# Performance work log

Hardware: AMD Instinct MI355X
Metric: run time of the kernel (lower is better)

The kernel has to match this reference:

```python
import jax, jax.numpy as jnp
import numpy as np
from jax import lax

DIM = 384
DIM_HEAD = 64
NUM_HEAD = DIM // DIM_HEAD
D_GROUPS = 3
NGD = DIM // D_GROUPS  # 128
KSIZE = 5
STRIDE = 2
PAD = KSIZE // 2
SCALE = DIM_HEAD ** -0.5
OFFSET_RANGE_FACTOR = 2.0
BN_EPS = 1e-6


def setup_inputs() -> dict:
    key = jax.random.key(0)
    ks = jax.random.split(key, 8)
    B, H, W = 8, 56, 56
    s = 0.02
    return {
        "x": jax.random.normal(ks[0], (B, DIM, H, W), jnp.float32),
        "q_w": jax.random.normal(ks[1], (DIM, DIM), jnp.float32) * s,
        "kv_w": jax.random.normal(ks[2], (2 * DIM, DIM), jnp.float32) * s,
        "proj_w": jax.random.normal(ks[3], (DIM, DIM), jnp.float32) * s,
        "proj_b": jnp.zeros((DIM,), jnp.float32),
        "dw_w": jax.random.normal(ks[4], (NGD, 1, KSIZE, KSIZE), jnp.float32) * s,
        "dw_b": jnp.zeros((NGD,), jnp.float32),
        "bn_w": jnp.ones((NGD,), jnp.float32),
        "bn_b": jnp.zeros((NGD,), jnp.float32),
        "bn_mean": jnp.zeros((NGD,), jnp.float32),
        "bn_var": jnp.ones((NGD,), jnp.float32),
        "pw_w": jax.random.normal(ks[5], (3, NGD), jnp.float32) * s,
    }


def grid_sample_bilinear(img, grid):
    # img: (N,C,H,W); grid: (N,Ho,Wo,2) with (x,y) in [-1,1]; align_corners=True, padding zeros
    N, C, H, W = img.shape
    gx = (grid[..., 0] + 1.0) * 0.5 * (W - 1)
    gy = (grid[..., 1] + 1.0) * 0.5 * (H - 1)
    x0 = jnp.floor(gx); y0 = jnp.floor(gy)
    x1 = x0 + 1.0; y1 = y0 + 1.0
    n_idx = jnp.arange(N)[:, None, None]

    def gather(yi, xi):
        valid = (yi >= 0) & (yi <= H - 1) & (xi >= 0) & (xi <= W - 1)
        yc = jnp.clip(yi, 0, H - 1).astype(jnp.int32)
        xc = jnp.clip(xi, 0, W - 1).astype(jnp.int32)
        v = img[n_idx, :, yc, xc]  # (N,Ho,Wo,C)
        return v * valid[..., None].astype(img.dtype)

    out = (gather(y0, x0) * ((x1 - gx) * (y1 - gy))[..., None]
           + gather(y1, x0) * ((x1 - gx) * (gy - y0))[..., None]
           + gather(y0, x1) * ((gx - x0) * (y1 - gy))[..., None]
           + gather(y1, x1) * ((gx - x0) * (gy - y0))[..., None])
    return out.transpose(0, 3, 1, 2)  # (N,C,Ho,Wo)


def _ref_points(H_off, W_off, n, dtype):
    ry = jnp.linspace(0.5, H_off - 0.5, H_off, dtype=dtype) / H_off * 2.0 - 1.0
    rx = jnp.linspace(0.5, W_off - 0.5, W_off, dtype=dtype) / W_off * 2.0 - 1.0
    ref = jnp.stack(jnp.meshgrid(ry, rx, indexing="ij"), -1)  # (Ho,Wo,2) as (y,x)
    return jnp.broadcast_to(ref[None], (n, H_off, W_off, 2))


def reference(x, q_w, kv_w, proj_w, proj_b, dw_w, dw_b, bn_w, bn_b, bn_mean, bn_var, pw_w):
    B, C, H, W = x.shape
    q = jnp.einsum("bchw,oc->bohw", x, q_w)  # 1x1 conv, no bias
    q_off = q.reshape(B * D_GROUPS, NGD, H, W)
    # depthwise conv (groups=NGD)
    off = lax.conv_general_dilated(q_off, dw_w, (STRIDE, STRIDE), [(PAD, PAD), (PAD, PAD)],
                                   feature_group_count=NGD,
                                   dimension_numbers=("NCHW", "OIHW", "NCHW"))
    off = off + dw_b[None, :, None, None]
    # BatchNorm2d (eval mode, running stats)
    off = (off - bn_mean[None, :, None, None]) * (bn_w / jnp.sqrt(bn_var + BN_EPS))[None, :, None, None] + bn_b[None, :, None, None]
    off = jax.nn.gelu(off, approximate=False)
    om = jnp.einsum("bchw,oc->bohw", off, pw_w)  # (Bg,3,Ho,Wo)
    offset, modulation = om[:, 0:2], jax.nn.sigmoid(om[:, 2:3])
    H_off, W_off = offset.shape[2], offset.shape[3]
    rng = jnp.array([1.0 / H_off, 1.0 / W_off], x.dtype).reshape(1, 2, 1, 1)
    offset = jnp.tanh(offset) * rng * OFFSET_RANGE_FACTOR
    offset = offset.transpose(0, 2, 3, 1)  # (Bg,Ho,Wo,2) as (y,x)
    pos = offset + _ref_points(H_off, W_off, B * D_GROUPS, x.dtype)
    grid = pos[..., ::-1]  # (x,y) for grid_sample
    x_s = grid_sample_bilinear(x.reshape(B * D_GROUPS, NGD, H, W), grid)
    x_s = x_s * jax.nn.sigmoid(modulation)  # note: double sigmoid as in source
    x_s = x_s.reshape(B, DIM, H_off, W_off)
    # attention
    qh = q.reshape(B, NUM_HEAD, DIM_HEAD, H * W).transpose(0, 1, 3, 2)  # (B,h,HW,d)
    kv = jnp.einsum("bchw,oc->bohw", x_s, kv_w)
    L = H_off * W_off
    kv = kv.reshape(B, 2, NUM_HEAD, DIM_HEAD, L).transpose(1, 0, 2, 4, 3)  # (2,B,h,L,d)
    k, v = kv[0], kv[1]
    attn = jax.nn.softmax(jnp.einsum("bhqd,bhkd->bhqk", qh, k) * SCALE, axis=-1)
    out = jnp.einsum("bhqk,bhkd->bhqd", attn, v)  # (B,h,HW,d)
    out = out.transpose(0, 1, 3, 2).reshape(B, DIM, H, W)
    out = jnp.einsum("bchw,oc->bohw", out, proj_w) + proj_b[None, :, None, None]
    return out
```

## Files before the change

### kernel.cpp

```cpp
#include <hip/hip_runtime.h>
#include <math.h>

#define DIMX 384
#define NHEAD 6
#define DHEAD 64
#define HW 3136
#define LKV 784
#define NGDX 128
#define NGRP 24

typedef __bf16 bf16_t;
typedef __bf16 bf16x4 __attribute__((ext_vector_type(4)));
typedef __bf16 bf16x8 __attribute__((ext_vector_type(8)));
typedef float  f32x4  __attribute__((ext_vector_type(4)));

typedef unsigned int u32_g __attribute__((address_space(1)));
typedef unsigned int u32_l __attribute__((address_space(3)));

static __device__ __forceinline__ f32x4 mfma16(bf16x8 a, bf16x8 b, f32x4 c) {
  return __builtin_amdgcn_mfma_f32_16x16x32_bf16(a, b, c, 0, 0, 0);
}
static __device__ __forceinline__ void gload16(const void* g, void* l) {
  __builtin_amdgcn_global_load_lds((const u32_g*)g, (u32_l*)l, 16, 0, 0);
}

__global__ __launch_bounds__(256) void xt_cvt(
    const float* __restrict__ x, bf16_t* __restrict__ xt)
{
  const int p0 = blockIdx.x * 64, c0 = blockIdx.y * 64, b = blockIdx.z;
  __shared__ float T[64][65];
  const int tid = threadIdx.x;
  {
    const int c = tid >> 2, pc = (tid & 3) * 16;
    const float* src = x + ((size_t)b * DIMX + c0 + c) * HW + p0 + pc;
#pragma unroll
    for (int j = 0; j < 4; ++j) {
      const float4 v = *(const float4*)(src + j * 4);
      T[c][pc + j * 4 + 0] = v.x; T[c][pc + j * 4 + 1] = v.y;
      T[c][pc + j * 4 + 2] = v.z; T[c][pc + j * 4 + 3] = v.w;
    }
  }
  __syncthreads();
  {
    const int p = tid >> 2, cc = (tid & 3) * 16;
    bf16_t* dst = xt + ((size_t)b * HW + p0 + p) * DIMX + c0 + cc;
#pragma unroll
    for (int jj = 0; jj < 2; ++jj) {
      bf16x8 o;
#pragma unroll
      for (int k = 0; k < 8; ++k) o[k] = (bf16_t)T[cc + jj * 8 + k][p];
      *(bf16x8*)(dst + jj * 8) = o;
    }
  }
}

__global__ __launch_bounds__(256) void cvt_w3(
    const float* __restrict__ qw, const float* __restrict__ kvw,
    const float* __restrict__ pw, bf16_t* __restrict__ dst)
{
  const int i = blockIdx.x * 256 + threadIdx.x;
  if (i >= 147456) return;
  const int e = i * 4;
  const float* src;
  int off;
  if (e < 147456)      { src = qw;  off = e; }
  else if (e < 442368) { src = kvw; off = e - 147456; }
  else                 { src = pw;  off = e - 442368; }
  const float4 v = *(const float4*)(src + off);
  bf16x4 o;
  o[0] = (bf16_t)v.x; o[1] = (bf16_t)v.y; o[2] = (bf16_t)v.z; o[3] = (bf16_t)v.w;
  *(bf16x4*)(dst + e) = o;
}

template<bool BIAS, bool OBF16>
__global__ __launch_bounds__(256) void gemm_qo(
    const bf16_t* __restrict__ W, const bf16_t* __restrict__ in,
    const float* __restrict__ bias, void* __restrict__ outv,
    int C, int P, int O)
{
  const int blk = blockIdx.x;
  const int y   = blk / 392;
  const int xb  = blk % 392;
  const int b   = xb / 49;
  const int o0  = y * 64;
  const int p0  = (xb % 49) * 64;
  __shared__ __align__(16) char smem[32768];
  const int tid = threadIdx.x;
  const int w = tid >> 6, lane = tid & 63, l15 = lane & 15, g = lane >> 4;
  const int lrow = lane >> 3;
  const int j    = lane & 7;

  const bf16_t* gA = W + (size_t)(o0 + w * 16 + lrow) * C + (j ^ lrow) * 8;
  const bf16_t* gB = in + ((size_t)b * P + p0 + w * 16 + lrow) * C + (j ^ lrow) * 8;

  f32x4 acc[4];
#pragma unroll
  for (int n = 0; n < 4; ++n) { acc[n][0]=0.f; acc[n][1]=0.f; acc[n][2]=0.f; acc[n][3]=0.f; }

  gload16(gA,         smem + w * 2048);
  gload16(gA + 8 * C, smem + w * 2048 + 1024);
  gload16(gB,         smem + 8192 + w * 2048);
  gload16(gB + 8 * C, smem + 8192 + w * 2048 + 1024);

  const int NK = C >> 6;
  for (int it = 0; it < NK; ++it) {
    const int buf = (it & 1) * 16384;
    __syncthreads();
    if (it + 1 < NK) {
      const int c1 = (it + 1) * 64;
      const int nb = ((it + 1) & 1) * 16384;
      gload16(gA + c1,         smem + nb + w * 2048);
      gload16(gA + c1 + 8 * C, smem + nb + w * 2048 + 1024);
      gload16(gB + c1,         smem + nb + 8192 + w * 2048);
      gload16(gB + c1 + 8 * C, smem + nb + 8192 + w * 2048 + 1024);
    }
#pragma unroll
    for (int ks = 0; ks < 2; ++ks) {
      const int cx = (ks * 64 + g * 16) ^ ((l15 & 7) << 4);
      const bf16x8 af = *(const bf16x8*)(smem + buf + (w * 16 + l15) * 128 + cx);
#pragma unroll
      for (int n = 0; n < 4; ++n) {
        const bf16x8 bfr = *(const bf16x8*)(smem + buf + 8192 + (n * 16 + l15) * 128 + cx);
        acc[n] = mfma16(af, bfr, acc[n]);
      }
    }
  }

  float badd[4];
#pragma unroll
  for (int r = 0; r < 4; ++r) badd[r] = BIAS ? bias[o0 + w * 16 + g * 4 + r] : 0.f;
#pragma unroll
  for (int n = 0; n < 4; ++n) {
    const int p = p0 + n * 16 + l15;
#pragma unroll
    for (int r = 0; r < 4; ++r) {
      const int o = o0 + w * 16 + g * 4 + r;
      const float v = acc[n][r] + badd[r];
      if (OBF16) ((bf16_t*)outv)[((size_t)b * O + o) * P + p] = (bf16_t)v;
      else       ((float*)outv)[((size_t)b * O + o) * P + p] = v;
    }
  }
}

__global__ __launch_bounds__(256) void gemm_kv(
    const bf16_t* __restrict__ W, const bf16_t* __restrict__ in,
    bf16_t* __restrict__ ktb, bf16_t* __restrict__ vtb, int C, int P, int O)
{
  const int b  = blockIdx.z;
  const int o0 = blockIdx.y * 64;
  const int p0 = blockIdx.x * 64;
  __shared__ __align__(16) bf16_t As[64][72];
  __shared__ __align__(16) bf16_t Bs[64][72];
  const int tid = threadIdx.x;
  const int w = tid >> 6, lane = tid & 63, l15 = lane & 15, g = lane >> 4;

  f32x4 acc[4];
#pragma unroll
  for (int n = 0; n < 4; ++n) { acc[n][0]=0.f; acc[n][1]=0.f; acc[n][2]=0.f; acc[n][3]=0.f; }

  for (int c0 = 0; c0 < C; c0 += 64) {
    {
      const int o = tid >> 2, cc = (tid & 3) * 16;
      const bf16_t* src = W + (size_t)(o0 + o) * C + c0 + cc;
      *(bf16x8*)&As[o][cc]     = *(const bf16x8*)src;
      *(bf16x8*)&As[o][cc + 8] = *(const bf16x8*)(src + 8);
    }
    {
      const int c = tid >> 2, pp = (tid & 3) * 16;
      const bf16_t* src = in + ((size_t)b * C + c0 + c) * P + p0 + pp;
#pragma unroll
      for (int jj = 0; jj < 2; ++jj) {
        bf16x8 v;
        if (p0 + pp + jj * 8 + 8 <= P) v = *(const bf16x8*)(src + jj * 8);
        else {
#pragma unroll
          for (int k = 0; k < 8; ++k) v[k] = (bf16_t)0.f;
        }
#pragma unroll
        for (int k = 0; k < 8; ++k) Bs[pp + jj * 8 + k][c] = v[k];
      }
    }
    __syncthreads();
#pragma unroll
    for (int ks = 0; ks < 2; ++ks) {
      const bf16x8 af = *(const bf16x8*)&As[w * 16 + l15][ks * 32 + g * 8];
#pragma unroll
      for (int n = 0; n < 4; ++n) {
        const bf16x8 bfr = *(const bf16x8*)&Bs[n * 16 + l15][ks * 32 + g * 8];
        acc[n] = mfma16(af, bfr, acc[n]);
      }
    }
    __syncthreads();
  }

  if (blockIdx.y < 6) {
    const int h = blockIdx.y;
#pragma unroll
    for (int n = 0; n < 4; ++n) {
      const int l = p0 + n * 16 + l15;
      if (l < P) {
        bf16x4 kq;
#pragma unroll
        for (int r = 0; r < 4; ++r) kq[r] = (bf16_t)acc[n][r];
        *(bf16x4*)&ktb[(((size_t)b * NHEAD + h) * LKV + l) * DHEAD + w * 16 + g * 4] = kq;
      }
    }
  } else {
#pragma unroll
    for (int n = 0; n < 4; ++n) {
      const int p = p0 + n * 16 + l15;
      if (p < P) {
#pragma unroll
        for (int r = 0; r < 4; ++r) {
          const int c = o0 - DIMX + w * 16 + g * 4 + r;
          vtb[((size_t)b * DIMX + c) * LKV + p] = (bf16_t)acc[n][r];
        }
      }
    }
  }
}

__global__ __launch_bounds__(256) void dw_bn_gelu(
    const bf16_t* __restrict__ q, const float* __restrict__ dw_w,
    const float* __restrict__ dw_b, const float* __restrict__ bn_w,
    const float* __restrict__ bn_b, const float* __restrict__ bn_mean,
    const float* __restrict__ bn_var, float* __restrict__ off)
{
  __shared__ float pl[3136];
  const int nc = blockIdx.x;
  const int c  = nc & 127;
  const bf16_t* plane = q + (size_t)nc * HW;
  const int tid = threadIdx.x;

  for (int i = tid; i < 392; i += 256) {
    const bf16x8 v = *(const bf16x8*)(plane + i * 8);
    f32x4 a, bq;
#pragma unroll
    for (int k = 0; k < 4; ++k) { a[k] = (float)v[k]; bq[k] = (float)v[4 + k]; }
    *(f32x4*)&pl[i * 8]     = a;
    *(f32x4*)&pl[i * 8 + 4] = bq;
  }
  float w[25];
#pragma unroll
  for (int k = 0; k < 25; ++k) w[k] = dw_w[c * 25 + k];
  const float beta  = dw_b[c];
  const float scale = bn_w[c] * rsqrtf(bn_var[c] + 1e-6f);
  const float shift = bn_b[c] - bn_mean[c] * scale;
  __syncthreads();

  for (int p = tid; p < LKV; p += 256) {
    const int oy = p / 28, ox = p % 28;
    const int iy0 = oy * 2 - 2, ix0 = ox * 2 - 2;
    float s = 0.f;
#pragma unroll
    for (int ky = 0; ky < 5; ++ky) {
      const int y = iy0 + ky;
      if ((unsigned)y >= 56u) continue;
#pragma unroll
      for (int kx = 0; kx < 5; ++kx) {
        const int x = ix0 + kx;
        if ((unsigned)x >= 56u) continue;
        s += pl[y * 56 + x] * w[ky * 5 + kx];
      }
    }
    s = (s + beta) * scale + shift;
    const float g = 0.5f * s * (1.f + erff(s * 0.70710678118654752f));
    off[(size_t)nc * LKV + p] = g;
  }
}

__global__ __launch_bounds__(64) void om_grid(
    const float* __restrict__ off, const float* __restrict__ pw_w,
    float* __restrict__ gxy, float* __restrict__ modb)
{
  const int n  = blockIdx.y;
  const int lane = threadIdx.x;
  const int p  = blockIdx.x * 16 + (lane & 15);
  const int cs = lane >> 4;
  const float* base = off + (size_t)n * NGDX * LKV + p;
  float s0 = 0.f, s1 = 0.f, s2 = 0.f;
#pragma unroll 8
  for (int cc = 0; cc < 32; ++cc) {
    const int c = cs * 32 + cc;
    const float v = base[(size_t)c * LKV];
    s0 += v * pw_w[c];
    s1 += v * pw_w[128 + c];
    s2 += v * pw_w[256 + c];
  }
  s0 += __shfl_xor(s0, 16); s0 += __shfl_xor(s0, 32);
  s1 += __shfl_xor(s1, 16); s1 += __shfl_xor(s1, 32);
  s2 += __shfl_xor(s2, 16); s2 += __shfl_xor(s2, 32);
  if (cs == 0) {
    const float sig1 = 1.f / (1.f + expf(-s2));
    const float mod  = 1.f / (1.f + expf(-sig1));
    const float offy = tanhf(s0) * (2.f / 28.f);
    const float offx = tanhf(s1) * (2.f / 28.f);
    const int i = p / 28, j = p % 28;
    const float refy = ((i + 0.5f) / 28.f) * 2.f - 1.f;
    const float refx = ((j + 0.5f) / 28.f) * 2.f - 1.f;
    const float gy = (offy + refy + 1.f) * 0.5f * 55.f;
    const float gx = (offx + refx + 1.f) * 0.5f * 55.f;
    gxy[((size_t)n * LKV + p) * 2 + 0] = gx;
    gxy[((size_t)n * LKV + p) * 2 + 1] = gy;
    modb[(size_t)n * LKV + p] = mod;
  }
}

__global__ __launch_bounds__(256) void sample_mod(
    const float* __restrict__ x, const float* __restrict__ gxy,
    const float* __restrict__ modb, bf16_t* __restrict__ xs)
{
  const int nc = blockIdx.x;
  const int n  = nc >> 7;
  const float* img = x + (size_t)nc * HW;
  for (int p = threadIdx.x; p < LKV; p += 256) {
    const float gx = gxy[((size_t)n * LKV + p) * 2 + 0];
    const float gy = gxy[((size_t)n * LKV + p) * 2 + 1];
    const float x0f = floorf(gx), y0f = floorf(gy);
    const float wx1 = gx - x0f, wy1 = gy - y0f;
    const float wx0 = (x0f + 1.f) - gx, wy0 = (y0f + 1.f) - gy;
    const int ix0 = (int)x0f, iy0 = (int)y0f;
    const int ix1 = ix0 + 1,  iy1 = iy0 + 1;
    const bool vx0 = (ix0 >= 0) && (ix0 < 56), vx1 = (ix1 >= 0) && (ix1 < 56);
    const bool vy0 = (iy0 >= 0) && (iy0 < 56), vy1 = (iy1 >= 0) && (iy1 < 56);
    const int cx0 = min(max(ix0, 0), 55), cx1 = min(max(ix1, 0), 55);
    const int cy0 = min(max(iy0, 0), 55), cy1 = min(max(iy1, 0), 55);
    const float f00 = (vy0 && vx0) ? img[cy0 * 56 + cx0] : 0.f;
    const float f10 = (vy1 && vx0) ? img[cy1 * 56 + cx0] : 0.f;
    const float f01 = (vy0 && vx1) ? img[cy0 * 56 + cx1] : 0.f;
    const float f11 = (vy1 && vx1) ? img[cy1 * 56 + cx1] : 0.f;
    const float v = f00 * (wx0 * wy0) + f10 * (wx0 * wy1)
                  + f01 * (wx1 * wy0) + f11 * (wx1 * wy1);
    xs[(size_t)nc * LKV + p] = (bf16_t)(v * modb[(size_t)n * LKV + p]);
  }
}

__global__ __launch_bounds__(256, 3) void attn_mfma(
    const bf16_t* __restrict__ q, const bf16_t* __restrict__ kt,
    const bf16_t* __restrict__ vt, bf16_t* __restrict__ aot)
{
  const int blk = blockIdx.x;
  const int bh  = blk % 48;
  const int t25 = blk / 48;
  const int h   = bh % NHEAD;
  const int b   = bh / NHEAD;
  const int p0  = t25 * 128;

  __shared__ __align__(16) char smem[40960];
  float (*Os)[68] = (float (*)[68])(smem);

  const int tid  = threadIdx.x;
  const int w    = tid >> 6;
  const int lane = tid & 63;
  const int l15  = lane & 15;
  const int g    = lane >> 4;
  const int lrow = lane >> 3;
  const int j    = lane & 7;

  const bf16_t* qb = q  + (size_t)(b * DIMX + h * DHEAD) * HW;
  const bf16_t* kb = kt + ((size_t)(b * NHEAD + h) * LKV) * DHEAD;
  const bf16_t* vb = vt + (size_t)(b * DIMX + h * DHEAD) * LKV;

  const bf16_t* gK = kb + (size_t)(w * 16 + lrow) * DHEAD + (j ^ lrow) * 8;
  const bf16_t* gV = vb + (size_t)(w * 16 + lrow) * LKV + (j ^ lrow) * 8;

  const float QSCL = 0.18033688011112042f;
  bf16x8 qf[2][2];
#pragma unroll
  for (int rs = 0; rs < 2; ++rs) {
    const int p = p0 + w * 32 + rs * 16 + l15;
    const bool valid = p < HW;
#pragma unroll
    for (int c2 = 0; c2 < 2; ++c2)
#pragma unroll
      for (int i = 0; i < 8; ++i) {
        const int d = c2 * 32 + g * 8 + i;
        qf[rs][c2][i] = valid ? (bf16_t)((float)qb[(size_t)d * HW + p] * QSCL) : (bf16_t)0.f;
      }
  }
  bf16x8 ones;
#pragma unroll
  for (int i = 0; i < 8; ++i) ones[i] = (bf16_t)1.0f;

  f32x4 acc[2][4];
  f32x4 lacc[2];
#pragma unroll
  for (int rs = 0; rs < 2; ++rs) {
    lacc[rs][0]=0.f; lacc[rs][1]=0.f; lacc[rs][2]=0.f; lacc[rs][3]=0.f;
#pragma unroll
    for (int n = 0; n < 4; ++n) { acc[rs][n][0]=0.f; acc[rs][n][1]=0.f; acc[rs][n][2]=0.f; acc[rs][n][3]=0.f; }
  }

  gload16(gK,                    smem + w * 2048);
  gload16(gK + (size_t)8*DHEAD,  smem + w * 2048 + 1024);
  gload16(gV,                    smem + 8192 + w * 2048);
  gload16(gV + (size_t)8*LKV,    smem + 8192 + w * 2048 + 1024);

  for (int t = 0; t < 13; ++t) {
    const int l0  = t * 64;
    const int buf = (t & 1) * 16384;
    __syncthreads();
    if (t < 12) {
      const int l1 = t * 64 + 64;
      const int nb = ((t + 1) & 1) * 16384;
      gload16(gK + (size_t)l1 * DHEAD,       smem + nb + w * 2048);
      gload16(gK + (size_t)(l1 + 8) * DHEAD, smem + nb + w * 2048 + 1024);
      gload16(gV + l1,                       smem + nb + 8192 + w * 2048);
      gload16(gV + (size_t)8 * LKV + l1,     smem + nb + 8192 + w * 2048 + 1024);
    }

    f32x4 s[2][4];
    __builtin_amdgcn_s_setprio(1);
#pragma unroll
    for (int n = 0; n < 4; ++n) {
      const int row = n * 16 + l15;
      const int cx0 = (g * 16) ^ ((l15 & 7) << 4);
      const int cx1 = (64 + g * 16) ^ ((l15 & 7) << 4);
      const bf16x8 k0 = *(const bf16x8*)(smem + buf + row * 128 + cx0);
      const bf16x8 k1 = *(const bf16x8*)(smem + buf + row * 128 + cx1);
#pragma unroll
      for (int rs = 0; rs < 2; ++rs) {
        f32x4 z; z[0]=0.f; z[1]=0.f; z[2]=0.f; z[3]=0.f;
        z = mfma16(k0, qf[rs][0], z);
        z = mfma16(k1, qf[rs][1], z);
        s[rs][n] = z;
      }
    }
    __builtin_amdgcn_s_setprio(0);
    if (l0 + 64 > LKV) {
#pragma unroll
      for (int n = 0; n < 4; ++n)
#pragma unroll
        for (int r = 0; r < 4; ++r)
          if (l0 + n * 16 + g * 4 + r >= LKV) {
#pragma unroll
            for (int rs = 0; rs < 2; ++rs) s[rs][n][r] = -1e30f;
          }
    }

    const int prow  = w * 16 + l15;
    char* pbase = smem + 32768 + prow * 128;
#pragma unroll
    for (int rs = 0; rs < 2; ++rs) {
#pragma unroll
      for (int n = 0; n < 4; ++n) {
        bf16x4 pk;
#pragma unroll
        for (int r = 0; r < 4; ++r) pk[r] = (bf16_t)exp2f(s[rs][n][r]);
        *(bf16x4*)(pbase + ((n * 32 + g * 8) ^ ((l15 & 7) << 4))) = pk;
      }
      __builtin_amdgcn_s_setprio(1);
#pragma unroll
      for (int c2 = 0; c2 < 2; ++c2) {
        bf16x8 vf[4];
#pragma unroll
        for (int n = 0; n < 4; ++n) {
          const int row = n * 16 + l15;
          const int cx = (c2 * 64 + g * 16) ^ ((l15 & 7) << 4);
          vf[n] = *(const bf16x8*)(smem + 8192 + buf + row * 128 + cx);
        }
        const bf16x8 pf = *(const bf16x8*)(pbase + ((c2 * 64 + g * 16) ^ ((l15 & 7) << 4)));
        lacc[rs] = mfma16(ones, pf, lacc[rs]);
#pragma unroll
        for (int n = 0; n < 4; ++n)
          acc[rs][n] = mfma16(vf[n], pf, acc[rs][n]);
      }
      __builtin_amdgcn_s_setprio(0);
    }
  }
  __syncthreads();

#pragma unroll
  for (int rs = 0; rs < 2; ++rs) {
    const float inv = 1.f / lacc[rs][0];
#pragma unroll
    for (int n = 0; n < 4; ++n) {
      f32x4 o4;
#pragma unroll
      for (int r = 0; r < 4; ++r) o4[r] = acc[rs][n][r] * inv;
      *(f32x4*)&Os[w * 32 + rs * 16 + l15][n * 16 + g * 4] = o4;
    }
  }
  __syncthreads();
  {
    const int pr = tid >> 1, c0 = (tid & 1) * 32;
    const int p = p0 + pr;
    if (p < HW) {
      bf16_t* dst = aot + ((size_t)b * HW + p) * DIMX + h * DHEAD + c0;
#pragma unroll
      for (int jj = 0; jj < 4; ++jj) {
        const f32x4 a = *(const f32x4*)&Os[pr][c0 + jj * 8];
        const f32x4 bq = *(const f32x4*)&Os[pr][c0 + jj * 8 + 4];
        bf16x8 o8;
        o8[0]=(bf16_t)a[0]; o8[1]=(bf16_t)a[1]; o8[2]=(bf16_t)a[2]; o8[3]=(bf16_t)a[3];
        o8[4]=(bf16_t)bq[0]; o8[5]=(bf16_t)bq[1]; o8[6]=(bf16_t)bq[2]; o8[7]=(bf16_t)bq[3];
        *(bf16x8*)(dst + jj * 8) = o8;
      }
    }
  }
}

extern "C" void kernel_launch(void* const* d_in, const int* in_sizes, int n_in,
                              void* d_out, int out_size, void* d_ws, size_t ws_size,
                              hipStream_t stream) {
  const float* x       = (const float*)d_in[0];
  const float* q_w     = (const float*)d_in[1];
  const float* kv_w    = (const float*)d_in[2];
  const float* proj_w  = (const float*)d_in[3];
  const float* proj_b  = (const float*)d_in[4];
  const float* dw_w    = (const float*)d_in[5];
  const float* dw_b    = (const float*)d_in[6];
  const float* bn_w    = (const float*)d_in[7];
  const float* bn_b    = (const float*)d_in[8];
  const float* bn_mean = (const float*)d_in[9];
  const float* bn_var  = (const float*)d_in[10];
  const float* pw_w    = (const float*)d_in[11];
  float* out = (float*)d_out;

  char* ws = (char*)d_ws;
  bf16_t* qbufb = (bf16_t*)(ws);
  float*  offb  = (float*)(ws + 19267584);
  float*  gxy   = (float*)(ws + 28901376);
  float*  modb  = (float*)(ws + 29051904);
  bf16_t* ktb   = (bf16_t*)(ws + 29127168);
  bf16_t* vtb   = (bf16_t*)(ws + 33944064);
  bf16_t* xsb   = (bf16_t*)(ws + 38760960);
  bf16_t* xt    = (bf16_t*)(ws + 43577856);
  bf16_t* aot   = xt;
  bf16_t* wbf   = (bf16_t*)(ws + 62845440);
  bf16_t* q_wb  = wbf;
  bf16_t* kv_wb = wbf + 147456;
  bf16_t* pj_wb = wbf + 442368;

  const dim3 blk(256);
  xt_cvt<<<dim3(49, 6, 8), blk, 0, stream>>>(x, xt);
  cvt_w3<<<dim3(576), blk, 0, stream>>>(q_w, kv_w, proj_w, wbf);
  gemm_qo<false, true><<<dim3(2352), blk, 0, stream>>>(q_wb, xt, nullptr, qbufb, 384, 3136, 384);
  dw_bn_gelu<<<dim3(3072), blk, 0, stream>>>(qbufb, dw_w, dw_b, bn_w, bn_b, bn_mean, bn_var, offb);
  om_grid<<<dim3(49, 24), dim3(64), 0, stream>>>(offb, pw_w, gxy, modb);
  sample_mod<<<dim3(3072), blk, 0, stream>>>(x, gxy, modb, xsb);
  gemm_kv<<<dim3(13, 12, 8), blk, 0, stream>>>(kv_wb, xsb, ktb, vtb, 384, 784, 768);
  attn_mfma<<<dim3(1200), blk, 0, stream>>>(qbufb, ktb, vtb, aot);
  gemm_qo<true, false><<<dim3(2352), blk, 0, stream>>>(pj_wb, aot, proj_b, out, 384, 3136, 384);
}
```

Baseline: 160.4 us.

## Double attention block to 512 threads sharing K/V tiles; pad depthwise conv plane

The attention kernel now runs 512-thread blocks that each cover 256 query positions, so every K/V tile loaded into shared memory serves twice as many queries. This halves global K/V traffic per query and halves the grid size. The output staging now takes two passes through the Os buffer, and shared memory grows to 48KB. Separately, the depthwise conv stages a zero-padded 60x60 plane in shared memory, which removes the per-tap bounds checks at the cost of an extra zeroing pass and a second barrier.

```diff
diff --git a/kernel.cpp b/kernel.cpp
--- a/kernel.cpp
+++ b/kernel.cpp
@@ -226,20 +226,13 @@
     const float* __restrict__ bn_b, const float* __restrict__ bn_mean,
     const float* __restrict__ bn_var, float* __restrict__ off)
 {
-  __shared__ float pl[3136];
+  __shared__ float pl[3600];
   const int nc = blockIdx.x;
   const int c  = nc & 127;
   const bf16_t* plane = q + (size_t)nc * HW;
   const int tid = threadIdx.x;
 
-  for (int i = tid; i < 392; i += 256) {
-    const bf16x8 v = *(const bf16x8*)(plane + i * 8);
-    f32x4 a, bq;
-#pragma unroll
-    for (int k = 0; k < 4; ++k) { a[k] = (float)v[k]; bq[k] = (float)v[4 + k]; }
-    *(f32x4*)&pl[i * 8]     = a;
-    *(f32x4*)&pl[i * 8 + 4] = bq;
-  }
+  for (int i = tid; i < 3600; i += 256) pl[i] = 0.f;
   float w[25];
 #pragma unroll
   for (int k = 0; k < 25; ++k) w[k] = dw_w[c * 25 + k];
@@ -248,21 +241,23 @@
   const float shift = bn_b[c] - bn_mean[c] * scale;
   __syncthreads();
 
+  for (int i = tid; i < 392; i += 256) {
+    const bf16x8 v = *(const bf16x8*)(plane + i * 8);
+    const int y = i / 7, x0 = (i % 7) * 8;
+    float* dst = &pl[(y + 2) * 60 + 2 + x0];
+#pragma unroll
+    for (int k = 0; k < 8; ++k) dst[k] = (float)v[k];
+  }
+  __syncthreads();
+
   for (int p = tid; p < LKV; p += 256) {
     const int oy = p / 28, ox = p % 28;
-    const int iy0 = oy * 2 - 2, ix0 = ox * 2 - 2;
     float s = 0.f;
 #pragma unroll
-    for (int ky = 0; ky < 5; ++ky) {
-      const int y = iy0 + ky;
-      if ((unsigned)y >= 56u) continue;
-#pragma unroll
-      for (int kx = 0; kx < 5; ++kx) {
-        const int x = ix0 + kx;
-        if ((unsigned)x >= 56u) continue;
-        s += pl[y * 56 + x] * w[ky * 5 + kx];
-      }
-    }
+    for (int ky = 0; ky < 5; ++ky)
+#pragma unroll
+      for (int kx = 0; kx < 5; ++kx)
+        s += pl[(oy * 2 + ky) * 60 + ox * 2 + kx] * w[ky * 5 + kx];
     s = (s + beta) * scale + shift;
     const float g = 0.5f * s * (1.f + erff(s * 0.70710678118654752f));
     off[(size_t)nc * LKV + p] = g;
@@ -335,7 +330,7 @@
   }
 }
 
-__global__ __launch_bounds__(256, 3) void attn_mfma(
+__global__ __launch_bounds__(512, 4) void attn_mfma(
     const bf16_t* __restrict__ q, const bf16_t* __restrict__ kt,
     const bf16_t* __restrict__ vt, bf16_t* __restrict__ aot)
 {
@@ -344,9 +339,9 @@
   const int t25 = blk / 48;
   const int h   = bh % NHEAD;
   const int b   = bh / NHEAD;
-  const int p0  = t25 * 128;
-
-  __shared__ __align__(16) char smem[40960];
+  const int p0  = t25 * 256;
+
+  __shared__ __align__(16) char smem[49152];
   float (*Os)[68] = (float (*)[68])(smem);
 
   const int tid  = threadIdx.x;
@@ -361,8 +356,8 @@
   const bf16_t* kb = kt + ((size_t)(b * NHEAD + h) * LKV) * DHEAD;
   const bf16_t* vb = vt + (size_t)(b * DIMX + h * DHEAD) * LKV;
 
-  const bf16_t* gK = kb + (size_t)(w * 16 + lrow) * DHEAD + (j ^ lrow) * 8;
-  const bf16_t* gV = vb + (size_t)(w * 16 + lrow) * LKV + (j ^ lrow) * 8;
+  const bf16_t* gK = kb + (size_t)(w * 8 + lrow) * DHEAD + (j ^ lrow) * 8;
+  const bf16_t* gV = vb + (size_t)(w * 8 + lrow) * LKV + (j ^ lrow) * 8;
 
   const float QSCL = 0.18033688011112042f;
   bf16x8 qf[2][2];
@@ -391,22 +386,18 @@
     for (int n = 0; n < 4; ++n) { acc[rs][n][0]=0.f; acc[rs][n][1]=0.f; acc[rs][n][2]=0.f; acc[rs][n][3]=0.f; }
   }
 
-  gload16(gK,                    smem + w * 2048);
-  gload16(gK + (size_t)8*DHEAD,  smem + w * 2048 + 1024);
-  gload16(gV,                    smem + 8192 + w * 2048);
-  gload16(gV + (size_t)8*LKV,    smem + 8192 + w * 2048 + 1024);
+  gload16(gK, smem + w * 1024);
+  gload16(gV, smem + 8192 + w * 1024);
 
   for (int t = 0; t < 13; ++t) {
     const int l0  = t * 64;
     const int buf = (t & 1) * 16384;
     __syncthreads();
     if (t < 12) {
-      const int l1 = t * 64 + 64;
+      const int l1 = l0 + 64;
       const int nb = ((t + 1) & 1) * 16384;
-      gload16(gK + (size_t)l1 * DHEAD,       smem + nb + w * 2048);
-      gload16(gK + (size_t)(l1 + 8) * DHEAD, smem + nb + w * 2048 + 1024);
-      gload16(gV + l1,                       smem + nb + 8192 + w * 2048);
-      gload16(gV + (size_t)8 * LKV + l1,     smem + nb + 8192 + w * 2048 + 1024);
+      gload16(gK + (size_t)l1 * DHEAD, smem + nb + w * 1024);
+      gload16(gV + l1,                 smem + nb + 8192 + w * 1024);
     }
 
     f32x4 s[2][4];
@@ -438,8 +429,7 @@
           }
     }
 
-    const int prow  = w * 16 + l15;
-    char* pbase = smem + 32768 + prow * 128;
+    char* pbase = smem + 32768 + (w * 16 + l15) * 128;
 #pragma unroll
     for (int rs = 0; rs < 2; ++rs) {
 #pragma unroll
@@ -470,33 +460,41 @@
   }
   __syncthreads();
 
-#pragma unroll
-  for (int rs = 0; rs < 2; ++rs) {
-    const float inv = 1.f / lacc[rs][0];
-#pragma unroll
-    for (int n = 0; n < 4; ++n) {
-      f32x4 o4;
-#pragma unroll
-      for (int r = 0; r < 4; ++r) o4[r] = acc[rs][n][r] * inv;
-      *(f32x4*)&Os[w * 32 + rs * 16 + l15][n * 16 + g * 4] = o4;
-    }
-  }
-  __syncthreads();
-  {
-    const int pr = tid >> 1, c0 = (tid & 1) * 32;
-    const int p = p0 + pr;
-    if (p < HW) {
-      bf16_t* dst = aot + ((size_t)b * HW + p) * DIMX + h * DHEAD + c0;
-#pragma unroll
-      for (int jj = 0; jj < 4; ++jj) {
-        const f32x4 a = *(const f32x4*)&Os[pr][c0 + jj * 8];
-        const f32x4 bq = *(const f32x4*)&Os[pr][c0 + jj * 8 + 4];
-        bf16x8 o8;
-        o8[0]=(bf16_t)a[0]; o8[1]=(bf16_t)a[1]; o8[2]=(bf16_t)a[2]; o8[3]=(bf16_t)a[3];
-        o8[4]=(bf16_t)bq[0]; o8[5]=(bf16_t)bq[1]; o8[6]=(bf16_t)bq[2]; o8[7]=(bf16_t)bq[3];
-        *(bf16x8*)(dst + jj * 8) = o8;
-      }
-    }
+  const int wl    = w & 3;
+  const int whalf = w >> 2;
+#pragma unroll
+  for (int pass = 0; pass < 2; ++pass) {
+    if (whalf == pass) {
+#pragma unroll
+      for (int rs = 0; rs < 2; ++rs) {
+        const float inv = 1.f / lacc[rs][0];
+#pragma unroll
+        for (int n = 0; n < 4; ++n) {
+          f32x4 o4;
+#pragma unroll
+          for (int r = 0; r < 4; ++r) o4[r] = acc[rs][n][r] * inv;
+          *(f32x4*)&Os[wl * 32 + rs * 16 + l15][n * 16 + g * 4] = o4;
+        }
+      }
+    }
+    __syncthreads();
+    {
+      const int pr = tid >> 2, c0 = (tid & 3) * 16;
+      const int p = p0 + pass * 128 + pr;
+      if (p < HW) {
+        bf16_t* dst = aot + ((size_t)b * HW + p) * DIMX + h * DHEAD + c0;
+#pragma unroll
+        for (int jj = 0; jj < 2; ++jj) {
+          const f32x4 a = *(const f32x4*)&Os[pr][c0 + jj * 8];
+          const f32x4 bq = *(const f32x4*)&Os[pr][c0 + jj * 8 + 4];
+          bf16x8 o8;
+          o8[0]=(bf16_t)a[0]; o8[1]=(bf16_t)a[1]; o8[2]=(bf16_t)a[2]; o8[3]=(bf16_t)a[3];
+          o8[4]=(bf16_t)bq[0]; o8[5]=(bf16_t)bq[1]; o8[6]=(bf16_t)bq[2]; o8[7]=(bf16_t)bq[3];
+          *(bf16x8*)(dst + jj * 8) = o8;
+        }
+      }
+    }
+    __syncthreads();
   }
 }
 
@@ -540,6 +538,6 @@
   om_grid<<<dim3(49, 24), dim3(64), 0, stream>>>(offb, pw_w, gxy, modb);
   sample_mod<<<dim3(3072), blk, 0, stream>>>(x, gxy, modb, xsb);
   gemm_kv<<<dim3(13, 12, 8), blk, 0, stream>>>(kv_wb, xsb, ktb, vtb, 384, 784, 768);
-  attn_mfma<<<dim3(1200), blk, 0, stream>>>(qbufb, ktb, vtb, aot);
+  attn_mfma<<<dim3(624), dim3(512), 0, stream>>>(qbufb, ktb, vtb, aot);
   gemm_qo<true, false><<<dim3(2352), blk, 0, stream>>>(pj_wb, aot, proj_b, out, 384, 3136, 384);
 }
```

Result: no change. 161.6 us (+0.8%).

## Fuse fp32-to-bf16 transpose of x into Q GEMM and pad depthwise conv plane

Applied to the files above, without the earlier changes.

Removes the separate xt_cvt kernel: the Q projection GEMM now reads fp32 x directly, converts it to bf16 and transposes it into shared memory per tile. This drops one kernel launch and a full write and read of the transposed bf16 copy of x. The new GEMM is not double-buffered and does scattered 2-byte LDS stores, so its inner loop may be slower, and each weight-row block re-reads and re-converts the fp32 x tile. Separately, the depthwise conv stages a zero-padded 60-wide plane so the 5x5 stencil loop needs no bounds checks.

```diff
diff --git a/kernel.cpp b/kernel.cpp
--- a/kernel.cpp
+++ b/kernel.cpp
@@ -22,36 +22,6 @@
 }
 static __device__ __forceinline__ void gload16(const void* g, void* l) {
   __builtin_amdgcn_global_load_lds((const u32_g*)g, (u32_l*)l, 16, 0, 0);
-}
-
-__global__ __launch_bounds__(256) void xt_cvt(
-    const float* __restrict__ x, bf16_t* __restrict__ xt)
-{
-  const int p0 = blockIdx.x * 64, c0 = blockIdx.y * 64, b = blockIdx.z;
-  __shared__ float T[64][65];
-  const int tid = threadIdx.x;
-  {
-    const int c = tid >> 2, pc = (tid & 3) * 16;
-    const float* src = x + ((size_t)b * DIMX + c0 + c) * HW + p0 + pc;
-#pragma unroll
-    for (int j = 0; j < 4; ++j) {
-      const float4 v = *(const float4*)(src + j * 4);
-      T[c][pc + j * 4 + 0] = v.x; T[c][pc + j * 4 + 1] = v.y;
-      T[c][pc + j * 4 + 2] = v.z; T[c][pc + j * 4 + 3] = v.w;
-    }
-  }
-  __syncthreads();
-  {
-    const int p = tid >> 2, cc = (tid & 3) * 16;
-    bf16_t* dst = xt + ((size_t)b * HW + p0 + p) * DIMX + c0 + cc;
-#pragma unroll
-    for (int jj = 0; jj < 2; ++jj) {
-      bf16x8 o;
-#pragma unroll
-      for (int k = 0; k < 8; ++k) o[k] = (bf16_t)T[cc + jj * 8 + k][p];
-      *(bf16x8*)(dst + jj * 8) = o;
-    }
-  }
 }
 
 __global__ __launch_bounds__(256) void cvt_w3(
@@ -72,10 +42,73 @@
   *(bf16x4*)(dst + e) = o;
 }
 
-template<bool BIAS, bool OBF16>
+__global__ __launch_bounds__(256) void gemm_q(
+    const bf16_t* __restrict__ W, const float* __restrict__ x,
+    bf16_t* __restrict__ outq)
+{
+  const int C = DIMX, P = HW, O = DIMX;
+  const int blk = blockIdx.x;
+  const int y   = blk / 392;
+  const int xb  = blk % 392;
+  const int b   = xb / 49;
+  const int o0  = y * 64;
+  const int p0  = (xb % 49) * 64;
+  __shared__ __align__(16) char smemA[8192];
+  __shared__ __align__(16) bf16_t Bs[64][72];
+  const int tid = threadIdx.x;
+  const int w = tid >> 6, lane = tid & 63, l15 = lane & 15, g = lane >> 4;
+  const int lrow = lane >> 3;
+  const int j    = lane & 7;
+
+  const bf16_t* gA = W + (size_t)(o0 + w * 16 + lrow) * C + (j ^ lrow) * 8;
+
+  f32x4 acc[4];
+#pragma unroll
+  for (int n = 0; n < 4; ++n) { acc[n][0]=0.f; acc[n][1]=0.f; acc[n][2]=0.f; acc[n][3]=0.f; }
+
+  for (int c0 = 0; c0 < C; c0 += 64) {
+    gload16(gA + c0,         smemA + w * 2048);
+    gload16(gA + c0 + 8 * C, smemA + w * 2048 + 1024);
+    {
+      const int c = tid >> 2, pp = (tid & 3) * 16;
+      const float* src = x + ((size_t)b * C + c0 + c) * HW + p0 + pp;
+#pragma unroll
+      for (int q4 = 0; q4 < 4; ++q4) {
+        const float4 v = *(const float4*)(src + q4 * 4);
+        Bs[pp + q4 * 4 + 0][c] = (bf16_t)v.x;
+        Bs[pp + q4 * 4 + 1][c] = (bf16_t)v.y;
+        Bs[pp + q4 * 4 + 2][c] = (bf16_t)v.z;
+        Bs[pp + q4 * 4 + 3][c] = (bf16_t)v.w;
+      }
+    }
+    __syncthreads();
+#pragma unroll
+    for (int ks = 0; ks < 2; ++ks) {
+      const int cx = (ks * 64 + g * 16) ^ ((l15 & 7) << 4);
+      const bf16x8 af = *(const bf16x8*)(smemA + (w * 16 + l15) * 128 + cx);
+#pragma unroll
+      for (int n = 0; n < 4; ++n) {
+        const bf16x8 bfr = *(const bf16x8*)&Bs[n * 16 + l15][ks * 32 + g * 8];
+        acc[n] = mfma16(af, bfr, acc[n]);
+      }
+    }
+    __syncthreads();
+  }
+
+#pragma unroll
+  for (int n = 0; n < 4; ++n) {
+    const int p = p0 + n * 16 + l15;
+#pragma unroll
+    for (int r = 0; r < 4; ++r) {
+      const int o = o0 + w * 16 + g * 4 + r;
+      outq[((size_t)b * O + o) * P + p] = (bf16_t)acc[n][r];
+    }
+  }
+}
+
 __global__ __launch_bounds__(256) void gemm_qo(
     const bf16_t* __restrict__ W, const bf16_t* __restrict__ in,
-    const float* __restrict__ bias, void* __restrict__ outv,
+    const float* __restrict__ bias, float* __restrict__ out,
     int C, int P, int O)
 {
   const int blk = blockIdx.x;
@@ -128,16 +161,14 @@
 
   float badd[4];
 #pragma unroll
-  for (int r = 0; r < 4; ++r) badd[r] = BIAS ? bias[o0 + w * 16 + g * 4 + r] : 0.f;
+  for (int r = 0; r < 4; ++r) badd[r] = bias[o0 + w * 16 + g * 4 + r];
 #pragma unroll
   for (int n = 0; n < 4; ++n) {
     const int p = p0 + n * 16 + l15;
 #pragma unroll
     for (int r = 0; r < 4; ++r) {
       const int o = o0 + w * 16 + g * 4 + r;
-      const float v = acc[n][r] + badd[r];
-      if (OBF16) ((bf16_t*)outv)[((size_t)b * O + o) * P + p] = (bf16_t)v;
-      else       ((float*)outv)[((size_t)b * O + o) * P + p] = v;
+      out[((size_t)b * O + o) * P + p] = acc[n][r] + badd[r];
     }
   }
 }
@@ -226,20 +257,13 @@
     const float* __restrict__ bn_b, const float* __restrict__ bn_mean,
     const float* __restrict__ bn_var, float* __restrict__ off)
 {
-  __shared__ float pl[3136];
+  __shared__ float pl[3600];
   const int nc = blockIdx.x;
   const int c  = nc & 127;
   const bf16_t* plane = q + (size_t)nc * HW;
   const int tid = threadIdx.x;
 
-  for (int i = tid; i < 392; i += 256) {
-    const bf16x8 v = *(const bf16x8*)(plane + i * 8);
-    f32x4 a, bq;
-#pragma unroll
-    for (int k = 0; k < 4; ++k) { a[k] = (float)v[k]; bq[k] = (float)v[4 + k]; }
-    *(f32x4*)&pl[i * 8]     = a;
-    *(f32x4*)&pl[i * 8 + 4] = bq;
-  }
+  for (int i = tid; i < 3600; i += 256) pl[i] = 0.f;
   float w[25];
 #pragma unroll
   for (int k = 0; k < 25; ++k) w[k] = dw_w[c * 25 + k];
@@ -248,21 +272,23 @@
   const float shift = bn_b[c] - bn_mean[c] * scale;
   __syncthreads();
 
+  for (int i = tid; i < 392; i += 256) {
+    const bf16x8 v = *(const bf16x8*)(plane + i * 8);
+    const int y = i / 7, x0 = (i % 7) * 8;
+    float* dst = &pl[(y + 2) * 60 + 2 + x0];
+#pragma unroll
+    for (int k = 0; k < 8; ++k) dst[k] = (float)v[k];
+  }
+  __syncthreads();
+
   for (int p = tid; p < LKV; p += 256) {
     const int oy = p / 28, ox = p % 28;
-    const int iy0 = oy * 2 - 2, ix0 = ox * 2 - 2;
     float s = 0.f;
 #pragma unroll
-    for (int ky = 0; ky < 5; ++ky) {
-      const int y = iy0 + ky;
-      if ((unsigned)y >= 56u) continue;
-#pragma unroll
-      for (int kx = 0; kx < 5; ++kx) {
-        const int x = ix0 + kx;
-        if ((unsigned)x >= 56u) continue;
-        s += pl[y * 56 + x] * w[ky * 5 + kx];
-      }
-    }
+    for (int ky = 0; ky < 5; ++ky)
+#pragma unroll
+      for (int kx = 0; kx < 5; ++kx)
+        s += pl[(oy * 2 + ky) * 60 + ox * 2 + kx] * w[ky * 5 + kx];
     s = (s + beta) * scale + shift;
     const float g = 0.5f * s * (1.f + erff(s * 0.70710678118654752f));
     off[(size_t)nc * LKV + p] = g;
@@ -525,21 +551,19 @@
   bf16_t* ktb   = (bf16_t*)(ws + 29127168);
   bf16_t* vtb   = (bf16_t*)(ws + 33944064);
   bf16_t* xsb   = (bf16_t*)(ws + 38760960);
-  bf16_t* xt    = (bf16_t*)(ws + 43577856);
-  bf16_t* aot   = xt;
+  bf16_t* aot   = (bf16_t*)(ws + 43577856);
   bf16_t* wbf   = (bf16_t*)(ws + 62845440);
   bf16_t* q_wb  = wbf;
   bf16_t* kv_wb = wbf + 147456;
   bf16_t* pj_wb = wbf + 442368;
 
   const dim3 blk(256);
-  xt_cvt<<<dim3(49, 6, 8), blk, 0, stream>>>(x, xt);
   cvt_w3<<<dim3(576), blk, 0, stream>>>(q_w, kv_w, proj_w, wbf);
-  gemm_qo<false, true><<<dim3(2352), blk, 0, stream>>>(q_wb, xt, nullptr, qbufb, 384, 3136, 384);
+  gemm_q<<<dim3(2352), blk, 0, stream>>>(q_wb, x, qbufb);
   dw_bn_gelu<<<dim3(3072), blk, 0, stream>>>(qbufb, dw_w, dw_b, bn_w, bn_b, bn_mean, bn_var, offb);
   om_grid<<<dim3(49, 24), dim3(64), 0, stream>>>(offb, pw_w, gxy, modb);
   sample_mod<<<dim3(3072), blk, 0, stream>>>(x, gxy, modb, xsb);
   gemm_kv<<<dim3(13, 12, 8), blk, 0, stream>>>(kv_wb, xsb, ktb, vtb, 384, 784, 768);
   attn_mfma<<<dim3(1200), blk, 0, stream>>>(qbufb, ktb, vtb, aot);
-  gemm_qo<true, false><<<dim3(2352), blk, 0, stream>>>(pj_wb, aot, proj_b, out, 384, 3136, 384);
-}
+  gemm_qo<<<dim3(2352), blk, 0, stream>>>(pj_wb, aot, proj_b, out, 384, 3136, 384);
+}
```

Measured after the change: 165.0 us. 2.9% more time.
